# Optimization experiments

Measured on AMD Instinct MI355X. Metric: run time of the kernel, lower is better.

## Reference

```python
import jax, jax.numpy as jnp
import numpy as np

EOS_TOKEN = 1


def _gru_cell(h, x, w_ih, w_hh, b_ih, b_hh):
    # PyTorch GRU cell. h, x: [B, H]; w_ih, w_hh: [3H, H]; b: [3H]
    gi = x @ w_ih.T + b_ih
    gh = h @ w_hh.T + b_hh
    i_r, i_z, i_n = jnp.split(gi, 3, axis=-1)
    h_r, h_z, h_n = jnp.split(gh, 3, axis=-1)
    r = jax.nn.sigmoid(i_r + h_r)
    z = jax.nn.sigmoid(i_z + h_z)
    n = jnp.tanh(i_n + r * h_n)
    return (1.0 - z) * n + z * h


def _mlp(y, w0, b0, w1, b1, w2, b2):
    # EncoderDNN(H, H, 1, 2): in_layer -> relu -> layer0 -> relu -> out_layer
    v = y @ w0.T + b0
    v = jax.nn.relu(v)
    v = v @ w1.T + b1
    v = jax.nn.relu(v)
    return v @ w2.T + b2  # [..., 1]


def setup_inputs() -> dict:
    key = jax.random.key(0)
    ks = jax.random.split(key, 16)
    B, L, H = 256, 256, 512
    STEM_V, TOK_V = 256, 128
    s = 1.0 / np.sqrt(H)
    u = lambda k, shape: jax.random.uniform(k, shape, jnp.float32, -s, s)
    return {
        "stem_batch": jax.random.randint(ks[0], (B,), 0, STEM_V),
        "goal_batch": jax.random.randint(ks[1], (B, L), 0, 123),
        "stem_emb": jax.random.normal(ks[2], (STEM_V, H), jnp.float32),
        "token_emb": jax.random.normal(ks[3], (TOK_V, H), jnp.float32),
        "w_ih": u(ks[4], (3 * H, H)),
        "w_hh": u(ks[5], (3 * H, H)),
        "b_ih": u(ks[6], (3 * H,)),
        "b_hh": u(ks[7], (3 * H,)),
        "w0": u(ks[8], (H, H)),
        "b0": u(ks[9], (H,)),
        "w1": u(ks[10], (H, H)),
        "b1": u(ks[11], (H,)),
        "w2": u(ks[12], (1, H)),
        "b2": u(ks[13], (1,)),
    }


def reference(stem_batch, goal_batch, stem_emb, token_emb,
              w_ih, w_hh, b_ih, b_hh, w0, b0, w1, b1, w2, b2):
    B, L = goal_batch.shape
    h0 = stem_emb[stem_batch]                         # [B, H]
    x_all = jax.nn.relu(token_emb[goal_batch])        # [B, L, H]
    x_tm = jnp.transpose(x_all, (1, 0, 2))            # [L, B, H] time-major

    def step(h, x):
        h_new = _gru_cell(h, x, w_ih, w_hh, b_ih, b_hh)
        return h_new, h_new

    h_last, hs = jax.lax.scan(step, h0, x_tm)         # hs: [L, B, H]
    lik = _mlp(jax.nn.relu(hs), w0, b0, w1, b1, w2, b2)  # [L, B, 1]

    x_eos = jax.nn.relu(jnp.broadcast_to(token_emb[EOS_TOKEN], (B, token_emb.shape[1])))
    h_final = _gru_cell(h_last, x_eos, w_ih, w_hh, b_ih, b_hh)
    final_lik = _mlp(jax.nn.relu(h_final), w0, b0, w1, b1, w2, b2)  # [B, 1]

    # original inserts the EOS-step likelihood at position 0, then cats on dim=1
    return jnp.concatenate([final_lik, jnp.transpose(lik[:, :, 0], (1, 0))], axis=1)  # [B, L+1]
```

## Files before the change

kernel.cpp:

```cpp
#include <hip/hip_runtime.h>
#include <math.h>

#define B 256
#define L 256
#define H 512
#define H3 1536
#define TOKV 128
#define EOS_TOK 1
#define OUTC 257
#define SLOT ((size_t)B * H)

typedef short s16;
typedef s16 s16x8 __attribute__((ext_vector_type(8)));
typedef s16 s16x4 __attribute__((ext_vector_type(4)));
typedef float f32x4v __attribute__((ext_vector_type(4)));
typedef unsigned long long u64;

__device__ __forceinline__ float sigmoidf_(float x) {
    return 1.0f / (1.0f + __expf(-x));
}

__device__ __forceinline__ s16 f2bf(float x) {
    unsigned u = __builtin_bit_cast(unsigned, x);
    u += 0x7fffu + ((u >> 16) & 1u);
    return (s16)(u >> 16);
}
__device__ __forceinline__ float bf2f(s16 h) {
    return __builtin_bit_cast(float, ((unsigned)(unsigned short)h) << 16);
}
__device__ __forceinline__ unsigned packsplit(float x) {
    s16 hh = f2bf(x);
    s16 ll = f2bf(x - bf2f(hh));
    return (unsigned)(unsigned short)hh | ((unsigned)(unsigned short)ll << 16);
}

__device__ __forceinline__ void clusterbar(unsigned* bar, int c, unsigned n, int tid) {
    __syncthreads();
    if (tid == 0) {
        const unsigned tgt = 32u * n;
        unsigned* ctr = bar + c * 32;
        asm volatile("" ::: "memory");
        __hip_atomic_fetch_add(ctr, 1u, __ATOMIC_RELAXED, __HIP_MEMORY_SCOPE_AGENT);
        while (__hip_atomic_load(ctr, __ATOMIC_RELAXED, __HIP_MEMORY_SCOPE_AGENT) < tgt)
            __builtin_amdgcn_s_sleep(1);
        asm volatile("" ::: "memory");
    }
    __syncthreads();
}

__global__ __launch_bounds__(256) void k_split(const float* __restrict__ src,
                                               s16* __restrict__ hi,
                                               s16* __restrict__ lo, int n4) {
    int i = blockIdx.x * 256 + threadIdx.x;
    if (i >= n4) return;
    float4 x = ((const float4*)src)[i];
    float xs[4] = {x.x, x.y, x.z, x.w};
    s16x4 h, l;
    #pragma unroll
    for (int q = 0; q < 4; ++q) {
        s16 hh = f2bf(xs[q]);
        h[q] = hh;
        l[q] = f2bf(xs[q] - bf2f(hh));
    }
    *(s16x4*)(hi + (size_t)i * 4) = h;
    *(s16x4*)(lo + (size_t)i * 4) = l;
}

__global__ __launch_bounds__(256) void k_gi_tok(
        const float* __restrict__ token_emb, const float* __restrict__ w_ih,
        const float* __restrict__ b_ih, float* __restrict__ gi_out) {
    __shared__ float wlds[96][132];
    __shared__ float elds[16][132];
    const int vi = blockIdx.x >> 4;
    const int ji = blockIdx.x & 15;
    const int v0 = vi << 4, j0 = ji * 96;
    const int tid = threadIdx.x;
    const int vl = tid & 7;
    const int jl = tid >> 3;
    float acc[2][3] = {{0.f, 0.f, 0.f}, {0.f, 0.f, 0.f}};
    for (int ck = 0; ck < 4; ++ck) {
        const int c0 = ck << 7;
        __syncthreads();
        for (int i = tid; i < 96 * 32; i += 256) {
            int row = i >> 5, c4 = i & 31;
            *(float4*)&wlds[row][c4 << 2] =
                *(const float4*)(w_ih + (size_t)(j0 + row) * H + c0 + (c4 << 2));
        }
        for (int i = tid; i < 16 * 32; i += 256) {
            int row = i >> 5, c4 = i & 31;
            float4 e = *(const float4*)(token_emb + (size_t)(v0 + row) * H + c0 + (c4 << 2));
            e.x = fmaxf(e.x, 0.f); e.y = fmaxf(e.y, 0.f);
            e.z = fmaxf(e.z, 0.f); e.w = fmaxf(e.w, 0.f);
            *(float4*)&elds[row][c4 << 2] = e;
        }
        __syncthreads();
        #pragma unroll 8
        for (int c = 0; c < 128; c += 4) {
            float4 wa = *(const float4*)&wlds[jl][c];
            float4 wb = *(const float4*)&wlds[32 + jl][c];
            float4 wc = *(const float4*)&wlds[64 + jl][c];
            float4 ea = *(const float4*)&elds[vl][c];
            float4 eb = *(const float4*)&elds[vl + 8][c];
            acc[0][0] += ea.x*wa.x + ea.y*wa.y + ea.z*wa.z + ea.w*wa.w;
            acc[0][1] += ea.x*wb.x + ea.y*wb.y + ea.z*wb.z + ea.w*wb.w;
            acc[0][2] += ea.x*wc.x + ea.y*wc.y + ea.z*wc.z + ea.w*wc.w;
            acc[1][0] += eb.x*wa.x + eb.y*wa.y + eb.z*wa.z + eb.w*wa.w;
            acc[1][1] += eb.x*wb.x + eb.y*wb.y + eb.z*wb.z + eb.w*wb.w;
            acc[1][2] += eb.x*wc.x + eb.y*wc.y + eb.z*wc.z + eb.w*wc.w;
        }
    }
    #pragma unroll
    for (int p = 0; p < 2; ++p) {
        int v = v0 + vl + (p << 3);
        #pragma unroll
        for (int s = 0; s < 3; ++s) {
            int j = j0 + (s << 5) + jl;
            gi_out[(size_t)v * H3 + j] = acc[p][s] + b_ih[j];
        }
    }
}

__global__ __launch_bounds__(128, 1) void k_scan(
        const int* __restrict__ goal, const int* __restrict__ stem,
        const float* __restrict__ stem_emb,
        const s16* __restrict__ w_hi, const s16* __restrict__ w_lo,
        const float* __restrict__ b_hh, const float* __restrict__ gi_tok,
        unsigned* __restrict__ spk0, unsigned* __restrict__ spk1,
        unsigned* __restrict__ hsp, unsigned* bar) {
    __shared__ s16 wlds[96 * 512];
    const int tid = threadIdx.x;
    const int wg = blockIdx.x;
    const int c = wg & 7;
    const int jt = wg >> 3;
    const int w = tid >> 6;
    const int l = tid & 63;
    const int ln = l & 15;
    const int kg = l >> 4;
    const int row0 = c * 32 + w * 16;
    const int j = jt * 16 + ln;

    for (int i = tid; i < 6144; i += 128) {
        int lane = i & 63;
        int chunk = i >> 6;
        int g2 = chunk >> 4;
        int kcIdx = chunk & 15;
        int gate = g2 >> 1, hl = g2 & 1;
        int lnn = lane & 15, kgg = lane >> 4;
        const s16* src = (hl ? w_lo : w_hi) +
                         ((size_t)(gate * H + jt * 16 + lnn)) * H + kcIdx * 32 + kgg * 8;
        *(s16x8*)(wlds + (size_t)i * 8) = *(const s16x8*)src;
    }
    {
        int b = c * 32 + jt;
        int blk = c * 2 + (jt >> 4);
        int lne = jt & 15;
        float4 v = ((const float4*)(stem_emb + (size_t)stem[b] * H))[tid];
        float xs[4] = {v.x, v.y, v.z, v.w};
        #pragma unroll
        for (int qq = 0; qq < 4; ++qq) {
            int col = tid * 4 + qq;
            int ku = col >> 1, s = col & 1;
            int ii = ku & 3, kgc = (ku >> 2) & 3, kc = ku >> 4;
            size_t slot = (size_t)blk * 8192 +
                          (size_t)(((kc * 4 + ii) * 64 + 16 * kgc + lne) * 2 + s);
            __hip_atomic_store(spk0 + slot, packsplit(xs[qq]),
                               __ATOMIC_RELAXED, __HIP_MEMORY_SCOPE_AGENT);
        }
    }
    float hprev[4];
    #pragma unroll
    for (int q = 0; q < 4; ++q) {
        int b = row0 + kg * 4 + q;
        hprev[q] = stem_emb[(size_t)stem[b] * H + j];
    }
    size_t wslot[4];
    {
        int ku = j >> 1, s = j & 1;
        int ii = ku & 3, kgc = (ku >> 2) & 3, kc = ku >> 4;
        size_t basef = (size_t)(c * 2 + w) * 8192 +
                       (size_t)(((kc * 4 + ii) * 64 + 16 * kgc) * 2 + s);
        #pragma unroll
        for (int q = 0; q < 4; ++q)
            wslot[q] = basef + (size_t)((kg * 4 + q) * 2);
    }
    clusterbar(bar, c, 1u, tid);

    const float bhr = b_hh[j], bhz = b_hh[H + j], bhn = b_hh[2 * H + j];

    for (int t = 0; t <= L; ++t) {
        unsigned* pin = (t & 1) ? spk1 : spk0;
        unsigned* pout = (t & 1) ? spk0 : spk1;
        unsigned* h_out = hsp + (size_t)(t < L ? t + 1 : 0) * SLOT;

        const u64* ap = (const u64*)pin + (size_t)(c * 2 + w) * 4096 + l;

        int bq[4];
        float g0[4], g1[4], g2v[4];
        #pragma unroll
        for (int q = 0; q < 4; ++q) {
            bq[q] = row0 + kg * 4 + q;
            int v = (t < L) ? goal[(size_t)bq[q] * L + t] : EOS_TOK;
            const float* gi = gi_tok + (size_t)v * H3;
            g0[q] = gi[j];
            g1[q] = gi[H + j];
            g2v[q] = gi[2 * H + j];
        }

        u64 av[64];
        #pragma unroll
        for (int kcii = 0; kcii < 64; ++kcii)
            av[kcii] = __hip_atomic_load(ap + (size_t)kcii * 64,
                                         __ATOMIC_RELAXED, __HIP_MEMORY_SCOPE_AGENT);

        f32x4v ar{}, az{}, an{};
        #pragma unroll
        for (int kcIdx = 0; kcIdx < 16; ++kcIdx) {
            s16x8 Ah, Al;
            #pragma unroll
            for (int i = 0; i < 4; ++i) {
                u64 wv = av[kcIdx * 4 + i];
                unsigned lo32 = (unsigned)wv, hi32 = (unsigned)(wv >> 32);
                Ah[2 * i]     = (s16)(lo32 & 0xffff);
                Al[2 * i]     = (s16)(lo32 >> 16);
                Ah[2 * i + 1] = (s16)(hi32 & 0xffff);
                Al[2 * i + 1] = (s16)(hi32 >> 16);
            }
            const s16* bb = wlds + ((size_t)(kcIdx * 64 + l)) * 8;
            s16x8 Rh = *(const s16x8*)(bb);
            s16x8 Rl = *(const s16x8*)(bb + 8192);
            s16x8 Zh = *(const s16x8*)(bb + 16384);
            s16x8 Zl = *(const s16x8*)(bb + 24576);
            s16x8 Nh = *(const s16x8*)(bb + 32768);
            s16x8 Nl = *(const s16x8*)(bb + 40960);
            ar = __builtin_amdgcn_mfma_f32_16x16x32_bf16(Ah, Rh, ar, 0, 0, 0);
            az = __builtin_amdgcn_mfma_f32_16x16x32_bf16(Ah, Zh, az, 0, 0, 0);
            an = __builtin_amdgcn_mfma_f32_16x16x32_bf16(Ah, Nh, an, 0, 0, 0);
            ar = __builtin_amdgcn_mfma_f32_16x16x32_bf16(Ah, Rl, ar, 0, 0, 0);
            az = __builtin_amdgcn_mfma_f32_16x16x32_bf16(Ah, Zl, az, 0, 0, 0);
            an = __builtin_amdgcn_mfma_f32_16x16x32_bf16(Ah, Nl, an, 0, 0, 0);
            ar = __builtin_amdgcn_mfma_f32_16x16x32_bf16(Al, Rh, ar, 0, 0, 0);
            az = __builtin_amdgcn_mfma_f32_16x16x32_bf16(Al, Zh, az, 0, 0, 0);
            an = __builtin_amdgcn_mfma_f32_16x16x32_bf16(Al, Nh, an, 0, 0, 0);
        }

        #pragma unroll
        for (int q = 0; q < 4; ++q) {
            float r = sigmoidf_(g0[q] + ar[q] + bhr);
            float z = sigmoidf_(g1[q] + az[q] + bhz);
            float x = g2v[q] + r * (an[q] + bhn);
            float e = __expf(-2.f * x);
            float nn = (1.f - e) / (1.f + e);
            float hn = (1.f - z) * nn + z * hprev[q];
            hprev[q] = hn;
            __builtin_nontemporal_store(packsplit(fmaxf(hn, 0.f)), h_out + wslot[q]);
            __hip_atomic_store(pout + wslot[q], packsplit(hn),
                               __ATOMIC_RELAXED, __HIP_MEMORY_SCOPE_AGENT);
        }

        if (t < L) clusterbar(bar, c, (unsigned)(t + 2), tid);
    }
}

__global__ __launch_bounds__(256, 1) void k_mlp_mfma(
        const unsigned* __restrict__ statesp,
        const s16* __restrict__ w0h, const s16* __restrict__ w0l,
        const float* __restrict__ b0v,
        const s16* __restrict__ w1h, const s16* __restrict__ w1l,
        const float* __restrict__ b1v,
        const float* __restrict__ w2v, const float* __restrict__ b2v,
        float* __restrict__ out, int col0) {
    __shared__ unsigned v1s[64 * 512];
    __shared__ float red[4][64];
    const int tid = threadIdx.x;
    const int wid = tid >> 6;
    const int l = tid & 63;
    const int ln = l & 15;
    const int kg = l >> 4;
    const int r0 = blockIdx.x * 64;
    const int col = col0 + (r0 >> 8);
    const int b0 = r0 & 255;
    const u64* slotb = (const u64*)statesp + (size_t)(r0 >> 8) * (SLOT / 2);
    const int blk0 = b0 >> 4;

    f32x4v acc[4][8];
    #pragma unroll
    for (int mf = 0; mf < 4; ++mf)
        #pragma unroll
        for (int nf = 0; nf < 8; ++nf) acc[mf][nf] = f32x4v{};

    for (int kc = 0; kc < H; kc += 32) {
        const int kcIdx = kc >> 5;
        s16x8 Ah[4], Al[4];
        #pragma unroll
        for (int mf = 0; mf < 4; ++mf) {
            const u64* sb = slotb + (size_t)(blk0 + mf) * 4096 + l;
            #pragma unroll
            for (int i = 0; i < 4; ++i) {
                u64 wv = sb[(size_t)(kcIdx * 4 + i) * 64];
                unsigned lo32 = (unsigned)wv, hi32 = (unsigned)(wv >> 32);
                Ah[mf][2 * i]     = (s16)(lo32 & 0xffff);
                Al[mf][2 * i]     = (s16)(lo32 >> 16);
                Ah[mf][2 * i + 1] = (s16)(hi32 & 0xffff);
                Al[mf][2 * i + 1] = (s16)(hi32 >> 16);
            }
        }
        #pragma unroll
        for (int nf = 0; nf < 8; ++nf) {
            const int n = wid * 128 + nf * 16 + ln;
            s16x8 Bh = *(const s16x8*)(w0h + (size_t)n * H + kc + kg * 8);
            s16x8 Bl = *(const s16x8*)(w0l + (size_t)n * H + kc + kg * 8);
            #pragma unroll
            for (int mf = 0; mf < 4; ++mf) {
                acc[mf][nf] = __builtin_amdgcn_mfma_f32_16x16x32_bf16(Ah[mf], Bh, acc[mf][nf], 0, 0, 0);
                acc[mf][nf] = __builtin_amdgcn_mfma_f32_16x16x32_bf16(Ah[mf], Bl, acc[mf][nf], 0, 0, 0);
                acc[mf][nf] = __builtin_amdgcn_mfma_f32_16x16x32_bf16(Al[mf], Bh, acc[mf][nf], 0, 0, 0);
            }
        }
    }
    float bn[8];
    #pragma unroll
    for (int nf = 0; nf < 8; ++nf) bn[nf] = b0v[wid * 128 + nf * 16 + ln];
    #pragma unroll
    for (int mf = 0; mf < 4; ++mf)
        #pragma unroll
        for (int nf = 0; nf < 8; ++nf)
            #pragma unroll
            for (int q = 0; q < 4; ++q) {
                int m = mf * 16 + kg * 4 + q;
                int n = wid * 128 + nf * 16 + ln;
                v1s[m * 512 + (n ^ ((m & 7) << 2))] = packsplit(fmaxf(acc[mf][nf][q] + bn[nf], 0.f));
            }
    __syncthreads();

    #pragma unroll
    for (int mf = 0; mf < 4; ++mf)
        #pragma unroll
        for (int nf = 0; nf < 8; ++nf) acc[mf][nf] = f32x4v{};
    for (int kc = 0; kc < H; kc += 32) {
        s16x8 Ah[4], Al[4];
        #pragma unroll
        for (int mf = 0; mf < 4; ++mf) {
            const int rr = mf * 16 + ln;
            const int cx = (rr & 7) << 2;
            const int k0 = kc + kg * 8;
            uint4 p0 = *(const uint4*)(v1s + rr * 512 + (k0 ^ cx));
            uint4 p1 = *(const uint4*)(v1s + rr * 512 + ((k0 + 4) ^ cx));
            unsigned pv[8] = {p0.x, p0.y, p0.z, p0.w, p1.x, p1.y, p1.z, p1.w};
            #pragma unroll
            for (int i = 0; i < 8; ++i) {
                Ah[mf][i] = (s16)(pv[i] & 0xffff);
                Al[mf][i] = (s16)(pv[i] >> 16);
            }
        }
        #pragma unroll
        for (int nf = 0; nf < 8; ++nf) {
            const int n = wid * 128 + nf * 16 + ln;
            s16x8 Bh = *(const s16x8*)(w1h + (size_t)n * H + kc + kg * 8);
            s16x8 Bl = *(const s16x8*)(w1l + (size_t)n * H + kc + kg * 8);
            #pragma unroll
            for (int mf = 0; mf < 4; ++mf) {
                acc[mf][nf] = __builtin_amdgcn_mfma_f32_16x16x32_bf16(Ah[mf], Bh, acc[mf][nf], 0, 0, 0);
                acc[mf][nf] = __builtin_amdgcn_mfma_f32_16x16x32_bf16(Ah[mf], Bl, acc[mf][nf], 0, 0, 0);
                acc[mf][nf] = __builtin_amdgcn_mfma_f32_16x16x32_bf16(Al[mf], Bh, acc[mf][nf], 0, 0, 0);
            }
        }
    }
    float b1n[8], w2n[8];
    #pragma unroll
    for (int nf = 0; nf < 8; ++nf) {
        int n = wid * 128 + nf * 16 + ln;
        b1n[nf] = b1v[n];
        w2n[nf] = w2v[n];
    }
    float psum[4][4];
    #pragma unroll
    for (int mf = 0; mf < 4; ++mf)
        #pragma unroll
        for (int q = 0; q < 4; ++q) {
            float s = 0.f;
            #pragma unroll
            for (int nf = 0; nf < 8; ++nf)
                s += fmaxf(acc[mf][nf][q] + b1n[nf], 0.f) * w2n[nf];
            psum[mf][q] = s;
        }
    #pragma unroll
    for (int mf = 0; mf < 4; ++mf)
        #pragma unroll
        for (int q = 0; q < 4; ++q) {
            float s = psum[mf][q];
            #pragma unroll
            for (int msk = 1; msk < 16; msk <<= 1)
                s += __shfl_xor(s, msk, 64);
            psum[mf][q] = s;
        }
    if (ln == 0) {
        #pragma unroll
        for (int mf = 0; mf < 4; ++mf)
            #pragma unroll
            for (int q = 0; q < 4; ++q)
                red[wid][mf * 16 + kg * 4 + q] = psum[mf][q];
    }
    __syncthreads();
    if (tid < 64) {
        float s = b2v[0] + red[0][tid] + red[1][tid] + red[2][tid] + red[3][tid];
        out[(size_t)(b0 + tid) * OUTC + col] = s;
    }
}

extern "C" void kernel_launch(void* const* d_in, const int* in_sizes, int n_in,
                              void* d_out, int out_size, void* d_ws, size_t ws_size,
                              hipStream_t stream) {
    (void)in_sizes; (void)n_in; (void)out_size; (void)ws_size;
    const int* stem = (const int*)d_in[0];
    const int* goal = (const int*)d_in[1];
    const float* stem_emb = (const float*)d_in[2];
    const float* token_emb = (const float*)d_in[3];
    const float* w_ih = (const float*)d_in[4];
    const float* w_hh = (const float*)d_in[5];
    const float* b_ih = (const float*)d_in[6];
    const float* b_hh = (const float*)d_in[7];
    const float* w0 = (const float*)d_in[8];
    const float* b0 = (const float*)d_in[9];
    const float* w1 = (const float*)d_in[10];
    const float* b1 = (const float*)d_in[11];
    const float* w2 = (const float*)d_in[12];
    const float* b2 = (const float*)d_in[13];
    float* out = (float*)d_out;

    char* p = (char*)d_ws;
    float* gi_tok = (float*)p;      p += (size_t)TOKV * H3 * 4;
    s16* whh_h = (s16*)p;           p += (size_t)H3 * H * 2;
    s16* whh_l = (s16*)p;           p += (size_t)H3 * H * 2;
    s16* w0h = (s16*)p;             p += (size_t)H * H * 2;
    s16* w0l = (s16*)p;             p += (size_t)H * H * 2;
    s16* w1h = (s16*)p;             p += (size_t)H * H * 2;
    s16* w1l = (s16*)p;             p += (size_t)H * H * 2;
    unsigned* spk0 = (unsigned*)p;  p += SLOT * 4;
    unsigned* spk1 = (unsigned*)p;  p += SLOT * 4;
    unsigned* bar = (unsigned*)p;   p += 4096;
    unsigned* hsp = (unsigned*)p;

    hipMemsetAsync(bar, 0, 4096, stream);

    k_split<<<768, 256, 0, stream>>>(w_hh, whh_h, whh_l, H3 * H / 4);
    k_split<<<256, 256, 0, stream>>>(w0, w0h, w0l, H * H / 4);
    k_split<<<256, 256, 0, stream>>>(w1, w1h, w1l, H * H / 4);
    k_gi_tok<<<128, 256, 0, stream>>>(token_emb, w_ih, b_ih, gi_tok);

    {
        const int* goal_a = goal;
        const int* stem_a = stem;
        const float* stem_emb_a = stem_emb;
        const s16* whh_h_a = whh_h;
        const s16* whh_l_a = whh_l;
        const float* b_hh_a = b_hh;
        const float* gi_tok_a = gi_tok;
        unsigned* spk0_a = spk0;
        unsigned* spk1_a = spk1;
        unsigned* hsp_a = hsp;
        unsigned* bar_a = bar;
        void* kargs[] = {(void*)&goal_a, (void*)&stem_a, (void*)&stem_emb_a,
                         (void*)&whh_h_a, (void*)&whh_l_a, (void*)&b_hh_a,
                         (void*)&gi_tok_a, (void*)&spk0_a, (void*)&spk1_a,
                         (void*)&hsp_a, (void*)&bar_a};
        hipError_t ce = hipLaunchCooperativeKernel((void*)k_scan, dim3(256),
                                                   dim3(128), kargs, 0, stream);
        if (ce != hipSuccess) {
            k_scan<<<256, 128, 0, stream>>>(goal, stem, stem_emb, whh_h, whh_l,
                                            b_hh, gi_tok, spk0, spk1, hsp, bar);
        }
    }

    k_mlp_mfma<<<1024, 256, 0, stream>>>(hsp + SLOT, w0h, w0l, b0,
                                         w1h, w1l, b1, w2, b2, out, 1);
    k_mlp_mfma<<<4, 256, 0, stream>>>(hsp, w0h, w0l, b0,
                                      w1h, w1l, b1, w2, b2, out, 0);
}
```

Baseline: 1.710 ms.

## Store each hidden state once in history buffer; stage through LDS for coalesced stores

The scan no longer writes two copies of each hidden state (a relu'd history copy plus a ping-pong exchange buffer). It writes a single packed hi/lo copy per timestep into the history buffer, which the next step reads directly. Output values are first staged through a small LDS buffer so each wave issues coalesced 64-bit atomic stores instead of scattered 32-bit ones. The ReLU moves into the MLP kernel's operand unpack, and the EOS-step state now sits at slot 257. This halves scan-side global writes at the cost of an extra LDS round-trip per step.

Result: faster. 1.658 ms (-3.1%).

```diff
diff --git a/kernel.cpp b/kernel.cpp
--- a/kernel.cpp
+++ b/kernel.cpp
@@ -32,6 +32,10 @@
     s16 hh = f2bf(x);
     s16 ll = f2bf(x - bf2f(hh));
     return (unsigned)(unsigned short)hh | ((unsigned)(unsigned short)ll << 16);
+}
+__device__ __forceinline__ unsigned relu_pk(unsigned pv) {
+    int m = ((int)(pv << 16)) >> 31;
+    return pv & ~(unsigned)m;
 }
 
 __device__ __forceinline__ void clusterbar(unsigned* bar, int c, unsigned n, int tid) {
@@ -125,9 +129,9 @@
         const float* __restrict__ stem_emb,
         const s16* __restrict__ w_hi, const s16* __restrict__ w_lo,
         const float* __restrict__ b_hh, const float* __restrict__ gi_tok,
-        unsigned* __restrict__ spk0, unsigned* __restrict__ spk1,
         unsigned* __restrict__ hsp, unsigned* bar) {
     __shared__ s16 wlds[96 * 512];
+    __shared__ unsigned stage[2][512];
     const int tid = threadIdx.x;
     const int wg = blockIdx.x;
     const int c = wg & 7;
@@ -163,7 +167,7 @@
             int ii = ku & 3, kgc = (ku >> 2) & 3, kc = ku >> 4;
             size_t slot = (size_t)blk * 8192 +
                           (size_t)(((kc * 4 + ii) * 64 + 16 * kgc + lne) * 2 + s);
-            __hip_atomic_store(spk0 + slot, packsplit(xs[qq]),
+            __hip_atomic_store(hsp + slot, packsplit(xs[qq]),
                                __ATOMIC_RELAXED, __HIP_MEMORY_SCOPE_AGENT);
         }
     }
@@ -173,26 +177,18 @@
         int b = row0 + kg * 4 + q;
         hprev[q] = stem_emb[(size_t)stem[b] * H + j];
     }
-    size_t wslot[4];
-    {
-        int ku = j >> 1, s = j & 1;
-        int ii = ku & 3, kgc = (ku >> 2) & 3, kc = ku >> 4;
-        size_t basef = (size_t)(c * 2 + w) * 8192 +
-                       (size_t)(((kc * 4 + ii) * 64 + 16 * kgc) * 2 + s);
-        #pragma unroll
-        for (int q = 0; q < 4; ++q)
-            wslot[q] = basef + (size_t)((kg * 4 + q) * 2);
-    }
     clusterbar(bar, c, 1u, tid);
 
     const float bhr = b_hh[j], bhz = b_hh[H + j], bhn = b_hh[2 * H + j];
+    const int ii2g = ((ln >> 1) & 3) * 2 + (ln >> 3);
+    const int sbit = ln & 1;
+    const size_t wavebase = (size_t)(c * 2 + w) * 4096 +
+                            (size_t)(jt >> 1) * 256 + (size_t)(jt & 1) * 32 + (l & 31);
 
     for (int t = 0; t <= L; ++t) {
-        unsigned* pin = (t & 1) ? spk1 : spk0;
-        unsigned* pout = (t & 1) ? spk0 : spk1;
-        unsigned* h_out = hsp + (size_t)(t < L ? t + 1 : 0) * SLOT;
-
-        const u64* ap = (const u64*)pin + (size_t)(c * 2 + w) * 4096 + l;
+        const int tau_out = (t < L) ? t + 1 : 257;
+        const u64* ap = (const u64*)hsp + (size_t)t * (SLOT / 2) +
+                        (size_t)(c * 2 + w) * 4096 + l;
 
         int bq[4];
         float g0[4], g1[4], g2v[4];
@@ -243,6 +239,7 @@
             an = __builtin_amdgcn_mfma_f32_16x16x32_bf16(Al, Nh, an, 0, 0, 0);
         }
 
+        unsigned pv[4];
         #pragma unroll
         for (int q = 0; q < 4; ++q) {
             float r = sigmoidf_(g0[q] + ar[q] + bhr);
@@ -252,9 +249,21 @@
             float nn = (1.f - e) / (1.f + e);
             float hn = (1.f - z) * nn + z * hprev[q];
             hprev[q] = hn;
-            __builtin_nontemporal_store(packsplit(fmaxf(hn, 0.f)), h_out + wslot[q]);
-            __hip_atomic_store(pout + wslot[q], packsplit(hn),
-                               __ATOMIC_RELAXED, __HIP_MEMORY_SCOPE_AGENT);
+            pv[q] = packsplit(hn);
+        }
+        {
+            unsigned* st = stage[w];
+            #pragma unroll
+            for (int q = 0; q < 4; ++q)
+                st[ii2g * 32 + (kg * 4 + q) * 2 + sbit] = pv[q];
+            const u64* stu = (const u64*)stage[w];
+            u64* outp = (u64*)hsp + (size_t)tau_out * (SLOT / 2) + wavebase;
+            #pragma unroll
+            for (int k = 0; k < 2; ++k) {
+                int iis = k * 2 + (l >> 5);
+                __hip_atomic_store(outp + (size_t)iis * 64, stu[iis * 32 + (l & 31)],
+                                   __ATOMIC_RELAXED, __HIP_MEMORY_SCOPE_AGENT);
+            }
         }
 
         if (t < L) clusterbar(bar, c, (unsigned)(t + 2), tid);
@@ -297,7 +306,8 @@
             #pragma unroll
             for (int i = 0; i < 4; ++i) {
                 u64 wv = sb[(size_t)(kcIdx * 4 + i) * 64];
-                unsigned lo32 = (unsigned)wv, hi32 = (unsigned)(wv >> 32);
+                unsigned lo32 = relu_pk((unsigned)wv);
+                unsigned hi32 = relu_pk((unsigned)(wv >> 32));
                 Ah[mf][2 * i]     = (s16)(lo32 & 0xffff);
                 Al[mf][2 * i]     = (s16)(lo32 >> 16);
                 Ah[mf][2 * i + 1] = (s16)(hi32 & 0xffff);
@@ -435,8 +445,6 @@
     s16* w0l = (s16*)p;             p += (size_t)H * H * 2;
     s16* w1h = (s16*)p;             p += (size_t)H * H * 2;
     s16* w1l = (s16*)p;             p += (size_t)H * H * 2;
-    unsigned* spk0 = (unsigned*)p;  p += SLOT * 4;
-    unsigned* spk1 = (unsigned*)p;  p += SLOT * 4;
     unsigned* bar = (unsigned*)p;   p += 4096;
     unsigned* hsp = (unsigned*)p;
 
@@ -455,24 +463,21 @@
         const s16* whh_l_a = whh_l;
         const float* b_hh_a = b_hh;
         const float* gi_tok_a = gi_tok;
-        unsigned* spk0_a = spk0;
-        unsigned* spk1_a = spk1;
         unsigned* hsp_a = hsp;
         unsigned* bar_a = bar;
         void* kargs[] = {(void*)&goal_a, (void*)&stem_a, (void*)&stem_emb_a,
                          (void*)&whh_h_a, (void*)&whh_l_a, (void*)&b_hh_a,
-                         (void*)&gi_tok_a, (void*)&spk0_a, (void*)&spk1_a,
-                         (void*)&hsp_a, (void*)&bar_a};
+                         (void*)&gi_tok_a, (void*)&hsp_a, (void*)&bar_a};
         hipError_t ce = hipLaunchCooperativeKernel((void*)k_scan, dim3(256),
                                                    dim3(128), kargs, 0, stream);
         if (ce != hipSuccess) {
             k_scan<<<256, 128, 0, stream>>>(goal, stem, stem_emb, whh_h, whh_l,
-                                            b_hh, gi_tok, spk0, spk1, hsp, bar);
+                                            b_hh, gi_tok, hsp, bar);
         }
     }
 
     k_mlp_mfma<<<1024, 256, 0, stream>>>(hsp + SLOT, w0h, w0l, b0,
                                          w1h, w1l, b1, w2, b2, out, 1);
-    k_mlp_mfma<<<4, 256, 0, stream>>>(hsp, w0h, w0l, b0,
+    k_mlp_mfma<<<4, 256, 0, stream>>>(hsp + (size_t)257 * SLOT, w0h, w0l, b0,
                                       w1h, w1l, b1, w2, b2, out, 0);
 }
```
